# Performance work log

Hardware: AMD Instinct MI355X
Metric: run time of the kernel (lower is better)

Reference implementation:

```python
import jax, jax.numpy as jnp
import numpy as np

EPS = 1e-5

def _graph_conv(x, src, dst, W, b, N):
    # DGL GraphConv, norm='both': D_out^{-1/2} then aggregate then D_in^{-1/2}
    ones = jnp.ones((src.shape[0],), x.dtype)
    out_deg = jnp.clip(jax.ops.segment_sum(ones, src, num_segments=N), 1.0)
    in_deg = jnp.clip(jax.ops.segment_sum(ones, dst, num_segments=N), 1.0)
    h = (x * (out_deg ** -0.5)[:, None]) @ W          # [N, out] (mult W before gather)
    agg = jax.ops.segment_sum(h[src], dst, num_segments=N)  # [N, out] irregular scatter
    return agg * (in_deg ** -0.5)[:, None] + b

def _bn_relu(h, gamma, beta):
    # BatchNorm1d in training mode: batch stats over node axis (biased var)
    mu = jnp.mean(h, axis=0)
    var = jnp.mean((h - mu) ** 2, axis=0)
    return jax.nn.relu((h - mu) * jax.lax.rsqrt(var + EPS) * gamma + beta)

def setup_inputs() -> dict:
    key = jax.random.key(0)
    ks = jax.random.split(key, 6)
    N, E, F, H, C = 100000, 1000000, 128, 128, 16
    return {
        "x": jax.random.normal(ks[0], (N, F), dtype=jnp.float32),
        "src": jax.random.randint(ks[1], (E,), 0, N, dtype=jnp.int32),
        "dst": jax.random.randint(ks[2], (E,), 0, N, dtype=jnp.int32),
        "W1": jax.random.normal(ks[3], (F, H), dtype=jnp.float32) * 0.05,
        "b1": jnp.zeros((H,), jnp.float32),
        "g1": jnp.ones((H,), jnp.float32),
        "be1": jnp.zeros((H,), jnp.float32),
        "W2": jax.random.normal(ks[4], (H, H), dtype=jnp.float32) * 0.05,
        "b2": jnp.zeros((H,), jnp.float32),
        "g2": jnp.ones((H,), jnp.float32),
        "be2": jnp.zeros((H,), jnp.float32),
        "Wc": jax.random.normal(ks[5], (H, C), dtype=jnp.float32) * 0.05,
        "bc": jnp.zeros((C,), jnp.float32),
    }

def reference(x, src, dst, W1, b1, g1, be1, W2, b2, g2, be2, Wc, bc):
    N = x.shape[0]
    h = _bn_relu(_graph_conv(x, src, dst, W1, b1, N), g1, be1)  # dropout = identity (eval)
    h = _bn_relu(_graph_conv(h, src, dst, W2, b2, N), g2, be2)
    return h @ Wc + bc  # [N, num_cls]
```

## Files before the change

### kernel.cpp

```cpp
#include <hip/hip_runtime.h>

#define FDIM 128
#define MAXDEG 64
#define GATHERB 2048
#define NREP 32

typedef unsigned short ushort_t;
typedef unsigned int uint_t;
typedef __attribute__((ext_vector_type(8))) short short8;
typedef __attribute__((ext_vector_type(16))) float float16;

__device__ __forceinline__ float bflo(uint_t u) { return __uint_as_float(u << 16); }
__device__ __forceinline__ float bfhi(uint_t u) { return __uint_as_float(u & 0xffff0000u); }
__device__ __forceinline__ ushort_t f2bf(float f) {
    uint_t u = __float_as_uint(f);
    return (ushort_t)((u + 0x7fffu + ((u >> 16) & 1u)) >> 16);
}
__device__ __forceinline__ uint_t pack2bf(float lo, float hi) {
    return (uint_t)f2bf(lo) | ((uint_t)f2bf(hi) << 16);
}

__global__ __launch_bounds__(256) void mega1_kernel(
    const float* __restrict__ x, const float* __restrict__ W,
    const int* __restrict__ src, const int* __restrict__ dst,
    int* __restrict__ cs, int* __restrict__ cursor, int* __restrict__ eidx,
    ushort_t* __restrict__ outb, int N, int E,
    int gemmB, int atomicB) {
    int bid = blockIdx.x;
    int t = threadIdx.x;

    int six = atomicB * 6;
    bool isAtomic;
    int idx;
    if (bid < six) {
        int grp = bid / 6, rem = bid % 6;
        if (rem == 5) { isAtomic = true; idx = grp; }
        else { isAtomic = false; idx = grp * 5 + rem; }
    } else {
        isAtomic = false;
        idx = atomicB * 5 + (bid - six);
    }

    if (isAtomic) {
        int stride = atomicB * 256;
        for (int i = idx * 256 + t; i < E; i += stride) {
            int d = dst[i];
            int s = src[i];
            int slot = atomicAdd(&cursor[d], 1);
            if (slot < MAXDEG) eidx[(size_t)d * MAXDEG + slot] = s;
            atomicAdd(&cs[s], 1);
        }
        return;
    }

    if (idx >= gemmB) return;
    __shared__ float xt[16][FDIM];
    int base = idx * 16;
    const float4* x4 = (const float4*)x;
#pragma unroll
    for (int i = 0; i < 2; i++) {
        int ii = t + i * 256;
        int row = ii >> 5, c4 = ii & 31;
        int grow = base + row;
        float4 v = make_float4(0.f, 0.f, 0.f, 0.f);
        if (grow < N) v = x4[(size_t)grow * 32 + c4];
        *(float4*)&xt[row][c4 * 4] = v;
    }
    __syncthreads();
    int rg = t >> 6, c = t & 63;
    float acc[4][2] = {};
    const float* Wc0 = W + c;
    for (int k4 = 0; k4 < 32; k4++) {
        float xv[16];
#pragma unroll
        for (int r = 0; r < 4; r++) {
            float4 tmp = *(const float4*)&xt[rg * 4 + r][k4 * 4];
            xv[r * 4 + 0] = tmp.x; xv[r * 4 + 1] = tmp.y;
            xv[r * 4 + 2] = tmp.z; xv[r * 4 + 3] = tmp.w;
        }
#pragma unroll
        for (int kk = 0; kk < 4; kk++) {
            float w0 = Wc0[(k4 * 4 + kk) * FDIM];
            float w1 = Wc0[(k4 * 4 + kk) * FDIM + 64];
#pragma unroll
            for (int r = 0; r < 4; r++) {
                acc[r][0] = fmaf(xv[r * 4 + kk], w0, acc[r][0]);
                acc[r][1] = fmaf(xv[r * 4 + kk], w1, acc[r][1]);
            }
        }
    }
#pragma unroll
    for (int r = 0; r < 4; r++) {
        int grow = base + rg * 4 + r;
        if (grow < N) {
            outb[(size_t)grow * FDIM + c] = f2bf(acc[r][0]);
            outb[(size_t)grow * FDIM + c + 64] = f2bf(acc[r][1]);
        }
    }
}

template <bool OS>
__global__ __launch_bounds__(256) void gather_kernel(const ushort_t* __restrict__ hb,
                                                     const int* __restrict__ eidx,
                                                     const int* __restrict__ cnt,
                                                     const int* __restrict__ cs,
                                                     const float* __restrict__ b,
                                                     ushort_t* __restrict__ outb,
                                                     float* __restrict__ statsRep, int N) {
    __shared__ float4 redS[256];
    __shared__ float4 redQ[256];
    int t = threadIdx.x;
    int wave = t >> 6, lane = t & 63;
    int half = lane >> 5, sub = lane & 31;
    int gw = blockIdx.x * 4 + wave;
    const uint2* h2 = (const uint2*)hb;
    uint2* o2 = (uint2*)outb;
    float4 bb = ((const float4*)b)[sub];
    float st0 = 0, st1 = 0, st2 = 0, st3 = 0, sq0 = 0, sq1 = 0, sq2 = 0, sq3 = 0;

    for (int node = gw; node < N; node += GATHERB * 4) {
        int deg = cnt[node];
        int e = min(deg, MAXDEG);
        const int* row = eidx + (size_t)node * MAXDEG;
        int ridx = (lane < e) ? row[lane] : 0;
        float scv = 1.f;
        if (OS) scv = (lane < e) ? rsqrtf((float)max(cs[ridx], 1)) : 0.f;

        float a0 = 0, a1 = 0, a2 = 0, a3 = 0;
        float c0 = 0, c1 = 0, c2 = 0, c3 = 0;
        int j = 0;
        for (; j + 3 < e; j += 4) {
            int iA = __shfl(ridx, j + half);
            int iB = __shfl(ridx, j + 2 + half);
            float sA = OS ? __shfl(scv, j + half) : 1.f;
            float sB = OS ? __shfl(scv, j + 2 + half) : 1.f;
            uint2 uA = h2[(size_t)iA * 32 + sub];
            uint2 uB = h2[(size_t)iB * 32 + sub];
            a0 = fmaf(bflo(uA.x), sA, a0); a1 = fmaf(bfhi(uA.x), sA, a1);
            a2 = fmaf(bflo(uA.y), sA, a2); a3 = fmaf(bfhi(uA.y), sA, a3);
            c0 = fmaf(bflo(uB.x), sB, c0); c1 = fmaf(bfhi(uB.x), sB, c1);
            c2 = fmaf(bflo(uB.y), sB, c2); c3 = fmaf(bfhi(uB.y), sB, c3);
        }
        for (; j < e; j += 2) {
            int jj = j + half;
            bool take = jj < e;
            int i0 = __shfl(ridx, take ? jj : (e - 1));
            float s0 = take ? (OS ? __shfl(scv, jj) : 1.f) : 0.f;
            uint2 u = h2[(size_t)i0 * 32 + sub];
            a0 = fmaf(bflo(u.x), s0, a0); a1 = fmaf(bfhi(u.x), s0, a1);
            a2 = fmaf(bflo(u.y), s0, a2); a3 = fmaf(bfhi(u.y), s0, a3);
        }
        a0 += c0; a1 += c1; a2 += c2; a3 += c3;
        a0 += __shfl_xor(a0, 32);
        a1 += __shfl_xor(a1, 32);
        a2 += __shfl_xor(a2, 32);
        a3 += __shfl_xor(a3, 32);
        if (half == 0) {
            float isc = rsqrtf((float)max(deg, 1));
            uint2 o;
            o.x = pack2bf(fmaf(a0, isc, bb.x), fmaf(a1, isc, bb.y));
            o.y = pack2bf(fmaf(a2, isc, bb.z), fmaf(a3, isc, bb.w));
            o2[(size_t)node * 32 + sub] = o;
            float v0 = bflo(o.x), v1 = bfhi(o.x), v2 = bflo(o.y), v3 = bfhi(o.y);
            st0 += v0; st1 += v1; st2 += v2; st3 += v3;
            sq0 = fmaf(v0, v0, sq0); sq1 = fmaf(v1, v1, sq1);
            sq2 = fmaf(v2, v2, sq2); sq3 = fmaf(v3, v3, sq3);
        }
    }

    redS[t] = make_float4(st0, st1, st2, st3);
    redQ[t] = make_float4(sq0, sq1, sq2, sq3);
    __syncthreads();
    if (t < 32) {
        float4 s = make_float4(0, 0, 0, 0), q = make_float4(0, 0, 0, 0);
#pragma unroll
        for (int w = 0; w < 4; w++) {
            float4 a = redS[w * 64 + t];
            float4 z = redQ[w * 64 + t];
            s.x += a.x; s.y += a.y; s.z += a.z; s.w += a.w;
            q.x += z.x; q.y += z.y; q.z += z.z; q.w += z.w;
        }
        float* dstp = statsRep + (size_t)(blockIdx.x & (NREP - 1)) * 256;
        atomicAdd(&dstp[t * 4 + 0], s.x);
        atomicAdd(&dstp[t * 4 + 1], s.y);
        atomicAdd(&dstp[t * 4 + 2], s.z);
        atomicAdd(&dstp[t * 4 + 3], s.w);
        atomicAdd(&dstp[128 + t * 4 + 0], q.x);
        atomicAdd(&dstp[128 + t * 4 + 1], q.y);
        atomicAdd(&dstp[128 + t * 4 + 2], q.z);
        atomicAdd(&dstp[128 + t * 4 + 3], q.w);
    }
}

__global__ __launch_bounds__(256) void gemm2_kernel(const ushort_t* __restrict__ hb,
                                                    const float* __restrict__ W,
                                                    const int* __restrict__ cs,
                                                    const float* __restrict__ statsRep,
                                                    const float* __restrict__ g,
                                                    const float* __restrict__ be,
                                                    ushort_t* __restrict__ outb, int N,
                                                    float invN) {
    __shared__ ushort_t zt[64][136];
    __shared__ ushort_t wt[128][136];
    __shared__ float Ash[FDIM], Bsh[FDIM];
    int t = threadIdx.x;
    int base = blockIdx.x * 64;

    if (t < FDIM) {
        float s = 0.f, q = 0.f;
        for (int r = 0; r < NREP; r++) {
            s += statsRep[r * 256 + t];
            q += statsRep[r * 256 + 128 + t];
        }
        float mu = s * invN;
        float var = q * invN - mu * mu;
        float a = g[t] * rsqrtf(var + 1e-5f);
        Ash[t] = a;
        Bsh[t] = be[t] - mu * a;
    }
    for (int i = t; i < FDIM * FDIM; i += 256) {
        int k = i >> 7, n = i & 127;
        wt[n][k] = f2bf(W[i]);
    }
    __syncthreads();

    const uint_t* h1 = (const uint_t*)hb;
    for (int i = t; i < 64 * 64; i += 256) {
        int row = i >> 6, cp = i & 63;
        int grow = base + row;
        uint_t o = 0;
        if (grow < N) {
            uint_t u = h1[(size_t)grow * 64 + cp];
            float s = rsqrtf((float)max(cs[grow], 1));
            float v0 = fmaxf(fmaf(bflo(u), Ash[cp * 2], Bsh[cp * 2]), 0.f) * s;
            float v1 = fmaxf(fmaf(bfhi(u), Ash[cp * 2 + 1], Bsh[cp * 2 + 1]), 0.f) * s;
            o = pack2bf(v0, v1);
        }
        *(uint_t*)&zt[row][cp * 2] = o;
    }
    __syncthreads();

    int wv = t >> 6, lane = t & 63;
    int rt = wv >> 1;
    int m = lane & 31;
    int kg = lane >> 5;

    short8 af[8];
#pragma unroll
    for (int kk = 0; kk < 8; kk++)
        af[kk] = *(const short8*)&zt[rt * 32 + m][kk * 16 + kg * 8];

#pragma unroll
    for (int cc = 0; cc < 2; cc++) {
        int ct = (wv & 1) * 2 + cc;
        float16 acc = {0, 0, 0, 0, 0, 0, 0, 0, 0, 0, 0, 0, 0, 0, 0, 0};
#pragma unroll
        for (int kk = 0; kk < 8; kk++) {
            short8 bf = *(const short8*)&wt[ct * 32 + m][kk * 16 + kg * 8];
            acc = __builtin_amdgcn_mfma_f32_32x32x16_bf16(af[kk], bf, acc, 0, 0, 0);
        }
        int col = ct * 32 + m;
#pragma unroll
        for (int r = 0; r < 16; r++) {
            int row = base + rt * 32 + (r & 3) + 8 * (r >> 2) + 4 * kg;
            if (row < N) outb[(size_t)row * FDIM + col] = f2bf(acc[r]);
        }
    }
}

__global__ __launch_bounds__(256) void cls_kernel(const ushort_t* __restrict__ hb,
                                                  const float* __restrict__ Wc,
                                                  const float* __restrict__ bc,
                                                  const float* __restrict__ statsRep,
                                                  const float* __restrict__ g,
                                                  const float* __restrict__ be,
                                                  float* __restrict__ out, int N, float invN) {
    __shared__ float wcl[FDIM * 16];
    __shared__ float red[16][256];
    __shared__ float Ash[FDIM], Bsh[FDIM];
    int t = threadIdx.x;
    int base = blockIdx.x * 64;
#pragma unroll
    for (int i = 0; i < 8; i++) wcl[t + i * 256] = Wc[t + i * 256];
    if (t < FDIM) {
        float s = 0.f, q = 0.f;
        for (int r = 0; r < NREP; r++) {
            s += statsRep[r * 256 + t];
            q += statsRep[r * 256 + 128 + t];
        }
        float mu = s * invN;
        float var = q * invN - mu * mu;
        float a = g[t] * rsqrtf(var + 1e-5f);
        Ash[t] = a;
        Bsh[t] = be[t] - mu * a;
    }
    __syncthreads();

    int node = base + (t >> 2);
    int q4 = t & 3;
    float acc[16];
#pragma unroll
    for (int c = 0; c < 16; c++) acc[c] = 0.f;

    if (node < N) {
        const uint2* hu2 = (const uint2*)((const uint_t*)hb + (size_t)node * 64 + q4 * 16);
        const float* Af = Ash + q4 * 32;
        const float* Bf = Bsh + q4 * 32;
#pragma unroll 1
        for (int kk = 0; kk < 8; kk++) {
            uint2 u = hu2[kk];
            float4 ab = *(const float4*)&Af[kk * 4];
            float4 bb = *(const float4*)&Bf[kk * 4];
            float v0 = fmaxf(fmaf(bflo(u.x), ab.x, bb.x), 0.f);
            float v1 = fmaxf(fmaf(bfhi(u.x), ab.y, bb.y), 0.f);
            float v2 = fmaxf(fmaf(bflo(u.y), ab.z, bb.z), 0.f);
            float v3 = fmaxf(fmaf(bfhi(u.y), ab.w, bb.w), 0.f);
            int k0 = q4 * 32 + kk * 4;
            const float* w0 = &wcl[k0 * 16];
#pragma unroll
            for (int c = 0; c < 16; c++) {
                float s = fmaf(v0, w0[c], fmaf(v1, w0[16 + c], fmaf(v2, w0[32 + c], v3 * w0[48 + c])));
                acc[c] += s;
            }
        }
    }
#pragma unroll
    for (int c = 0; c < 16; c++) red[c][t] = acc[c];
    __syncthreads();
#pragma unroll
    for (int i = t; i < 64 * 16; i += 256) {
        int n = i >> 4, c = i & 15;
        float4 p = *(const float4*)&red[c][n * 4];
        int grow = base + n;
        if (grow < N) out[(size_t)grow * 16 + c] = (p.x + p.y) + (p.z + p.w) + bc[c];
    }
}

extern "C" void kernel_launch(void* const* d_in, const int* in_sizes, int n_in,
                              void* d_out, int out_size, void* d_ws, size_t ws_size,
                              hipStream_t stream) {
    const float* x  = (const float*)d_in[0];
    const int* src  = (const int*)d_in[1];
    const int* dst  = (const int*)d_in[2];
    const float* W1 = (const float*)d_in[3];
    const float* b1 = (const float*)d_in[4];
    const float* g1 = (const float*)d_in[5];
    const float* be1= (const float*)d_in[6];
    const float* W2 = (const float*)d_in[7];
    const float* b2 = (const float*)d_in[8];
    const float* g2 = (const float*)d_in[9];
    const float* be2= (const float*)d_in[10];
    const float* Wc = (const float*)d_in[11];
    const float* bc = (const float*)d_in[12];
    float* out = (float*)d_out;

    int N = in_sizes[0] / FDIM;
    int E = in_sizes[1];
    size_t NB = (size_t)N * FDIM;

    ushort_t* bufA = (ushort_t*)d_ws;
    ushort_t* bufB = bufA + NB;
    int* cs        = (int*)(bufB + NB);
    int* cursor    = cs + N;
    float* statsR1 = (float*)(cursor + N);
    float* statsR2 = statsR1 + NREP * 256;
    int* eidx      = (int*)(statsR2 + NREP * 256);

    hipMemsetAsync(cs, 0, ((size_t)2 * N + 2 * NREP * 256) * sizeof(int), stream);

    int gemmB = (N + 15) / 16;
    int atomicB = (gemmB + 4) / 5;
    int totalB = gemmB + atomicB;

    mega1_kernel<<<totalB, 256, 0, stream>>>(
        x, W1, src, dst, cs, cursor, eidx, bufA, N, E, gemmB, atomicB);

    float invN = 1.0f / N;

    gather_kernel<true><<<GATHERB, 256, 0, stream>>>(bufA, eidx, cursor, cs, b1, bufB, statsR1, N);

    gemm2_kernel<<<(N + 63) / 64, 256, 0, stream>>>(bufB, W2, cs, statsR1, g1, be1, bufA, N, invN);
    gather_kernel<false><<<GATHERB, 256, 0, stream>>>(bufA, eidx, cursor, nullptr, b2, bufB, statsR2, N);

    cls_kernel<<<(N + 63) / 64, 256, 0, stream>>>(bufB, Wc, bc, statsR2, g2, be2, out, N, invN);
}
```

Before: 383.7 us.

## Build ELL adjacency with two-pass bucket sort instead of global atomics

Replaces the global-atomic scatter that built the per-destination edge list and source degree counts with a two-pass radix-style bucketing. The first kernel bins edges by a 128-node range in LDS per chunk. The second kernel assembles each range's ELL rows and degree counts in shared memory before writing them out coalesced. This targets the contention and random global writes of the atomic approach. In exchange, the GEMM is no longer overlapped with graph construction, and two extra launches are added. Fixed capacities (PCAP, RCAP) limit the edge and node counts it can handle.

After: 390.1 us. About the same (+1.7%).

```diff
diff --git a/kernel.cpp b/kernel.cpp
--- a/kernel.cpp
+++ b/kernel.cpp
@@ -4,6 +4,12 @@
 #define MAXDEG 64
 #define GATHERB 2048
 #define NREP 32
+
+#define RSIZE 128
+#define RSHIFT 7
+#define RCAP 1024
+#define CCAP 14336
+#define PCAP 80
 
 typedef unsigned short ushort_t;
 typedef unsigned int uint_t;
@@ -20,40 +26,11 @@
     return (uint_t)f2bf(lo) | ((uint_t)f2bf(hi) << 16);
 }
 
-__global__ __launch_bounds__(256) void mega1_kernel(
+__global__ __launch_bounds__(256) void gemm1_kernel(
     const float* __restrict__ x, const float* __restrict__ W,
-    const int* __restrict__ src, const int* __restrict__ dst,
-    int* __restrict__ cs, int* __restrict__ cursor, int* __restrict__ eidx,
-    ushort_t* __restrict__ outb, int N, int E,
-    int gemmB, int atomicB) {
-    int bid = blockIdx.x;
-    int t = threadIdx.x;
-
-    int six = atomicB * 6;
-    bool isAtomic;
-    int idx;
-    if (bid < six) {
-        int grp = bid / 6, rem = bid % 6;
-        if (rem == 5) { isAtomic = true; idx = grp; }
-        else { isAtomic = false; idx = grp * 5 + rem; }
-    } else {
-        isAtomic = false;
-        idx = atomicB * 5 + (bid - six);
-    }
-
-    if (isAtomic) {
-        int stride = atomicB * 256;
-        for (int i = idx * 256 + t; i < E; i += stride) {
-            int d = dst[i];
-            int s = src[i];
-            int slot = atomicAdd(&cursor[d], 1);
-            if (slot < MAXDEG) eidx[(size_t)d * MAXDEG + slot] = s;
-            atomicAdd(&cs[s], 1);
-        }
-        return;
-    }
-
-    if (idx >= gemmB) return;
+    ushort_t* __restrict__ outb, int N) {
+    int idx = blockIdx.x;
+    int t = threadIdx.x;
     __shared__ float xt[16][FDIM];
     int base = idx * 16;
     const float4* x4 = (const float4*)x;
@@ -96,6 +73,124 @@
             outb[(size_t)grow * FDIM + c] = f2bf(acc[r][0]);
             outb[(size_t)grow * FDIM + c + 64] = f2bf(acc[r][1]);
         }
+    }
+}
+
+__global__ __launch_bounds__(256) void bucket_kernel(
+    const int* __restrict__ src, const int* __restrict__ dst,
+    uint_t* __restrict__ bktD, int* __restrict__ baseD,
+    uint_t* __restrict__ bktS, int* __restrict__ baseS,
+    int E, int P, int R) {
+    __shared__ uint4 buf4[CCAP / 4];
+    __shared__ int hist[RCAP];
+    __shared__ int scanbuf[256];
+    uint_t* buf = (uint_t*)buf4;
+    int t = threadIdx.x;
+    int role = blockIdx.x >= P;
+    int p = role ? blockIdx.x - P : blockIdx.x;
+    const int* key = role ? src : dst;
+    int e0 = p * CCAP;
+    int e1 = min(E, e0 + CCAP);
+    int cnt = e1 - e0;
+
+    for (int r = t; r < R; r += 256) hist[r] = 0;
+    __syncthreads();
+    for (int i = e0 + t; i < e1; i += 256) atomicAdd(&hist[key[i] >> RSHIFT], 1);
+    __syncthreads();
+
+    int b0 = t * 4;
+    int hv[4];
+    int s0 = 0;
+#pragma unroll
+    for (int k = 0; k < 4; k++) {
+        hv[k] = (b0 + k < R) ? hist[b0 + k] : 0;
+        s0 += hv[k];
+    }
+    scanbuf[t] = s0;
+    __syncthreads();
+    for (int off = 1; off < 256; off <<= 1) {
+        int v = (t >= off) ? scanbuf[t - off] : 0;
+        __syncthreads();
+        scanbuf[t] += v;
+        __syncthreads();
+    }
+    int run = scanbuf[t] - s0;
+    int* baseG = role ? baseS : baseD;
+#pragma unroll
+    for (int k = 0; k < 4; k++) {
+        if (b0 + k < R) {
+            baseG[(b0 + k) * P + p] = run;
+            hist[b0 + k] = run;
+        }
+        run += hv[k];
+    }
+    if (t == 0) baseG[R * P + p] = cnt;
+    __syncthreads();
+
+    for (int i = e0 + t; i < e1; i += 256) {
+        int kv = key[i];
+        int slot = atomicAdd(&hist[kv >> RSHIFT], 1);
+        uint_t entry = role ? (uint_t)kv
+                            : (((uint_t)(kv & (RSIZE - 1)) << 25) | (uint_t)src[i]);
+        buf[slot] = entry;
+    }
+    __syncthreads();
+
+    uint_t* outp = role ? bktS : bktD;
+    uint4* og = (uint4*)(outp + (size_t)e0);
+    int n4 = (cnt + 3) >> 2;
+    for (int j = t; j < n4; j += 256) og[j] = buf4[j];
+}
+
+__global__ __launch_bounds__(256) void build_kernel(
+    const uint_t* __restrict__ bktD, const int* __restrict__ baseD,
+    const uint_t* __restrict__ bktS, const int* __restrict__ baseS,
+    int* __restrict__ eidx, int* __restrict__ cnt, int* __restrict__ cs,
+    int N, int P) {
+    __shared__ uint4 ell4[RSIZE][MAXDEG / 4];
+    __shared__ int cntN[RSIZE], csN[RSIZE];
+    __shared__ int dB0[PCAP], dB1[PCAP], sB0[PCAP], sB1[PCAP];
+    uint_t* ell = (uint_t*)ell4;
+    int t = threadIdx.x;
+    int r = blockIdx.x;
+
+    if (t < RSIZE) { cntN[t] = 0; csN[t] = 0; }
+    for (int i = t; i < P; i += 256) {
+        dB0[i] = baseD[r * P + i];
+        dB1[i] = baseD[(r + 1) * P + i];
+        sB0[i] = baseS[r * P + i];
+        sB1[i] = baseS[(r + 1) * P + i];
+    }
+    __syncthreads();
+
+    int wave = t >> 6, lane = t & 63;
+    for (int p = wave; p < P; p += 4) {
+        int b = dB0[p], len = dB1[p] - b;
+        const uint_t* seg = bktD + (size_t)p * CCAP + b;
+        for (int i = lane; i < len; i += 64) {
+            uint_t e = seg[i];
+            int dl = e >> 25;
+            uint_t s = e & 0x1FFFFFFu;
+            int slot = atomicAdd(&cntN[dl], 1);
+            if (slot < MAXDEG) ell[dl * MAXDEG + slot] = s;
+        }
+        int b2 = sB0[p], len2 = sB1[p] - b2;
+        const uint_t* seg2 = bktS + (size_t)p * CCAP + b2;
+        for (int i = lane; i < len2; i += 64)
+            atomicAdd(&csN[seg2[i] & (RSIZE - 1)], 1);
+    }
+    __syncthreads();
+
+    int base = r * RSIZE;
+    for (int i = t; i < RSIZE * (MAXDEG / 4); i += 256) {
+        int n = i >> 4, q = i & 15;
+        int g = base + n;
+        if (g < N && q * 4 < min(cntN[n], MAXDEG))
+            ((uint4*)eidx)[(size_t)g * (MAXDEG / 4) + q] = ell4[n][q];
+    }
+    if (t < RSIZE) {
+        int g = base + t;
+        if (g < N) { cnt[g] = cntN[t]; cs[g] = csN[t]; }
     }
 }
 
@@ -361,26 +456,33 @@
     ushort_t* bufA = (ushort_t*)d_ws;
     ushort_t* bufB = bufA + NB;
     int* cs        = (int*)(bufB + NB);
-    int* cursor    = cs + N;
-    float* statsR1 = (float*)(cursor + N);
+    int* cnt       = cs + N;
+    float* statsR1 = (float*)(cnt + N);
     float* statsR2 = statsR1 + NREP * 256;
     int* eidx      = (int*)(statsR2 + NREP * 256);
 
-    hipMemsetAsync(cs, 0, ((size_t)2 * N + 2 * NREP * 256) * sizeof(int), stream);
+    uint_t* bktD = (uint_t*)bufB;
+    uint_t* bktS = bktD + (size_t)PCAP * CCAP;
+    int* baseD   = (int*)(bktS + (size_t)PCAP * CCAP);
+    int* baseS   = baseD + (RCAP + 1) * PCAP;
+
+    int P = (E + CCAP - 1) / CCAP;
+    int R = (N + RSIZE - 1) >> RSHIFT;
+
+    hipMemsetAsync(statsR1, 0, (size_t)2 * NREP * 256 * sizeof(float), stream);
+
+    bucket_kernel<<<2 * P, 256, 0, stream>>>(src, dst, bktD, baseD, bktS, baseS, E, P, R);
+    build_kernel<<<R, 256, 0, stream>>>(bktD, baseD, bktS, baseS, eidx, cnt, cs, N, P);
 
     int gemmB = (N + 15) / 16;
-    int atomicB = (gemmB + 4) / 5;
-    int totalB = gemmB + atomicB;
-
-    mega1_kernel<<<totalB, 256, 0, stream>>>(
-        x, W1, src, dst, cs, cursor, eidx, bufA, N, E, gemmB, atomicB);
+    gemm1_kernel<<<gemmB, 256, 0, stream>>>(x, W1, bufA, N);
 
     float invN = 1.0f / N;
 
-    gather_kernel<true><<<GATHERB, 256, 0, stream>>>(bufA, eidx, cursor, cs, b1, bufB, statsR1, N);
+    gather_kernel<true><<<GATHERB, 256, 0, stream>>>(bufA, eidx, cnt, cs, b1, bufB, statsR1, N);
 
     gemm2_kernel<<<(N + 63) / 64, 256, 0, stream>>>(bufB, W2, cs, statsR1, g1, be1, bufA, N, invN);
-    gather_kernel<false><<<GATHERB, 256, 0, stream>>>(bufA, eidx, cursor, nullptr, b2, bufB, statsR2, N);
+    gather_kernel<false><<<GATHERB, 256, 0, stream>>>(bufA, eidx, cnt, nullptr, b2, bufB, statsR2, N);
 
     cls_kernel<<<(N + 63) / 64, 256, 0, stream>>>(bufB, Wc, bc, statsR2, g2, be2, out, N, invN);
 }
```
